# Optimization experiments

Hardware: AMD Instinct MI355X
Metric: run time of the kernel (lower is better)

Reference implementation:

```python
import jax, jax.numpy as jnp
import numpy as np

B, S, D = 64, 2048, 1024

def setup_inputs() -> dict:
    key = jax.random.key(0)
    k1, k2, k3 = jax.random.split(key, 3)
    enc_mask = jax.random.randint(k1, (B, S), 0, 2).astype(bool)  # True = masked (padding)
    enc_out = jax.random.normal(k2, (B, S, D), dtype=jnp.float32)
    dec_hid = jax.random.normal(k3, (B, D), dtype=jnp.float32)
    return {"enc_mask": enc_mask, "enc_out": enc_out, "dec_hid": dec_hid}

def reference(enc_mask, enc_out, dec_hid):
    # scores: [B, S] = dot(enc_out[b,s,:], dec_hid[b,:])
    sims = jnp.einsum('bsd,bd->bs', enc_out, dec_hid)
    sims = jnp.where(enc_mask, -jnp.inf, sims)
    attention = jax.nn.softmax(sims, axis=1)          # [B, S]
    context = jnp.einsum('bs,bsd->bd', attention, enc_out)  # [B, D]
    return context
```

## Files before the change

### kernel.cpp

```cpp
#include <hip/hip_runtime.h>
#include <math.h>


constexpr int Bc = 64;
constexpr int Sc = 2048;
constexpr int Dc = 1024;

__global__ __launch_bounds__(256, 4)
void attn_partial(const int* __restrict__ mask,
                  const float* __restrict__ enc,
                  const float* __restrict__ hid,
                  float* __restrict__ o_part,
                  float* __restrict__ ml_part,
                  float* __restrict__ out_final,
                  int SPLIT, int CHUNK)
{
    __shared__ float so[4][Dc];
    __shared__ float sm[4], sl[4];

    const int split = blockIdx.x;
    const int b     = blockIdx.y;
    const int tid   = threadIdx.x;
    const int wid   = tid >> 6;
    const int lane  = tid & 63;
    const int d0    = lane << 2;

    const float* hb = hid + (size_t)b * Dc;
    const float4 h0 = *(const float4*)(hb + d0);
    const float4 h1 = *(const float4*)(hb + d0 + 256);
    const float4 h2 = *(const float4*)(hb + d0 + 512);
    const float4 h3 = *(const float4*)(hb + d0 + 768);

    float4 o0 = make_float4(0.f,0.f,0.f,0.f);
    float4 o1 = o0, o2 = o0, o3 = o0;
    float m = -INFINITY, l = 0.f;

    const int rpw  = CHUNK >> 2;
    const int sbeg = split * CHUNK + wid * rpw;
    const int* mrow = mask + (size_t)b * Sc;
    const float* ebase = enc + ((size_t)b * Sc + (size_t)sbeg) * Dc;

    for (int i = 0; i < rpw; ++i) {
        if (mrow[sbeg + i]) continue;
        const float* row = ebase + (size_t)i * Dc;
        const float4 x0 = *(const float4*)(row + d0);
        const float4 x1 = *(const float4*)(row + d0 + 256);
        const float4 x2 = *(const float4*)(row + d0 + 512);
        const float4 x3 = *(const float4*)(row + d0 + 768);

        float p = x0.x*h0.x + x0.y*h0.y + x0.z*h0.z + x0.w*h0.w;
        p      += x1.x*h1.x + x1.y*h1.y + x1.z*h1.z + x1.w*h1.w;
        p      += x2.x*h2.x + x2.y*h2.y + x2.z*h2.z + x2.w*h2.w;
        p      += x3.x*h3.x + x3.y*h3.y + x3.z*h3.z + x3.w*h3.w;
        #pragma unroll
        for (int off = 32; off > 0; off >>= 1)
            p += __shfl_xor(p, off, 64);

        const float mn = fmaxf(m, p);
        const float a  = __expf(m - mn);
        const float w  = __expf(p - mn);
        l = l * a + w;
        m = mn;
        o0.x = o0.x*a + w*x0.x;  o0.y = o0.y*a + w*x0.y;
        o0.z = o0.z*a + w*x0.z;  o0.w = o0.w*a + w*x0.w;
        o1.x = o1.x*a + w*x1.x;  o1.y = o1.y*a + w*x1.y;
        o1.z = o1.z*a + w*x1.z;  o1.w = o1.w*a + w*x1.w;
        o2.x = o2.x*a + w*x2.x;  o2.y = o2.y*a + w*x2.y;
        o2.z = o2.z*a + w*x2.z;  o2.w = o2.w*a + w*x2.w;
        o3.x = o3.x*a + w*x3.x;  o3.y = o3.y*a + w*x3.y;
        o3.z = o3.z*a + w*x3.z;  o3.w = o3.w*a + w*x3.w;
    }

    if (lane == 0) { sm[wid] = m; sl[wid] = l; }
    *(float4*)&so[wid][d0      ] = o0;
    *(float4*)&so[wid][d0 + 256] = o1;
    *(float4*)&so[wid][d0 + 512] = o2;
    *(float4*)&so[wid][d0 + 768] = o3;
    __syncthreads();

    const float M  = fmaxf(fmaxf(sm[0], sm[1]), fmaxf(sm[2], sm[3]));
    const float e0 = __expf(sm[0] - M);
    const float e1 = __expf(sm[1] - M);
    const float e2 = __expf(sm[2] - M);
    const float e3 = __expf(sm[3] - M);
    const float L  = sl[0]*e0 + sl[1]*e1 + sl[2]*e2 + sl[3]*e3;

    const int dd = tid << 2;
    const float4 v0 = *(float4*)&so[0][dd];
    const float4 v1 = *(float4*)&so[1][dd];
    const float4 v2 = *(float4*)&so[2][dd];
    const float4 v3 = *(float4*)&so[3][dd];
    float4 acc;
    acc.x = v0.x*e0 + v1.x*e1 + v2.x*e2 + v3.x*e3;
    acc.y = v0.y*e0 + v1.y*e1 + v2.y*e2 + v3.y*e3;
    acc.z = v0.z*e0 + v1.z*e1 + v2.z*e2 + v3.z*e3;
    acc.w = v0.w*e0 + v1.w*e1 + v2.w*e2 + v3.w*e3;

    if (out_final) {
        const float inv = (L > 0.f) ? 1.f / L : 0.f;
        acc.x *= inv; acc.y *= inv; acc.z *= inv; acc.w *= inv;
        *(float4*)&out_final[(size_t)b * Dc + dd] = acc;
    } else {
        *(float4*)&o_part[((size_t)b * SPLIT + split) * Dc + dd] = acc;
        if (tid == 0) {
            ml_part[((size_t)b * SPLIT + split) * 2    ] = M;
            ml_part[((size_t)b * SPLIT + split) * 2 + 1] = L;
        }
    }
}

__global__ __launch_bounds__(256)
void attn_combine(const float* __restrict__ o_part,
                  const float* __restrict__ ml_part,
                  float* __restrict__ out, int SPLIT)
{
    __shared__ float sme[64], sle[64];
    const int b   = blockIdx.x;
    const int tid = threadIdx.x;
    if (tid < SPLIT) {
        sme[tid] = ml_part[((size_t)b * SPLIT + tid) * 2];
        sle[tid] = ml_part[((size_t)b * SPLIT + tid) * 2 + 1];
    }
    __syncthreads();

    float M = -INFINITY;
    for (int s = 0; s < SPLIT; ++s) M = fmaxf(M, sme[s]);
    float L = 0.f;
    for (int s = 0; s < SPLIT; ++s) L += sle[s] * __expf(sme[s] - M);

    const int dd = tid << 2;
    float4 acc = make_float4(0.f,0.f,0.f,0.f);
    for (int s = 0; s < SPLIT; ++s) {
        const float e = __expf(sme[s] - M);
        const float4 v = *(const float4*)&o_part[((size_t)b * SPLIT + s) * Dc + dd];
        acc.x += e * v.x; acc.y += e * v.y; acc.z += e * v.z; acc.w += e * v.w;
    }
    const float inv = (L > 0.f) ? 1.f / L : 0.f;
    acc.x *= inv; acc.y *= inv; acc.z *= inv; acc.w *= inv;
    *(float4*)&out[(size_t)b * Dc + dd] = acc;
}

extern "C" void kernel_launch(void* const* d_in, const int* in_sizes, int n_in,
                              void* d_out, int out_size, void* d_ws, size_t ws_size,
                              hipStream_t stream)
{
    const int*   mask = (const int*)d_in[0];
    const float* enc  = (const float*)d_in[1];
    const float* hid  = (const float*)d_in[2];
    float*       out  = (float*)d_out;

    int SPLIT = 32;
    while (SPLIT > 1 &&
           (size_t)Bc * SPLIT * (Dc + 2) * sizeof(float) > ws_size)
        SPLIT >>= 1;
    const bool direct =
        (SPLIT == 1) || ((size_t)Bc * (Dc + 2) * sizeof(float) > ws_size);
    if (direct) SPLIT = 1;

    float* o_part  = (float*)d_ws;
    float* ml_part = o_part + (size_t)Bc * SPLIT * Dc;

    attn_partial<<<dim3(SPLIT, Bc), 256, 0, stream>>>(
        mask, enc, hid,
        direct ? nullptr : o_part,
        direct ? nullptr : ml_part,
        direct ? out : nullptr,
        SPLIT, Sc / SPLIT);

    if (!direct)
        attn_combine<<<Bc, 256, 0, stream>>>(o_part, ml_part, out, SPLIT);
}
```

Baseline: 644.6 us.

## Batch four unmasked rows per iteration using ballot-compacted mask

After: 644.9 us. No clear change (+0.1%).

```diff
diff --git a/kernel.cpp b/kernel.cpp
--- a/kernel.cpp
+++ b/kernel.cpp
@@ -6,7 +6,19 @@
 constexpr int Sc = 2048;
 constexpr int Dc = 1024;
 
-__global__ __launch_bounds__(256, 4)
+__device__ __forceinline__ float dot16(const float4& a, const float4& b,
+                                       const float4& c, const float4& d,
+                                       const float4& h0, const float4& h1,
+                                       const float4& h2, const float4& h3)
+{
+    float p = a.x*h0.x + a.y*h0.y + a.z*h0.z + a.w*h0.w;
+    p      += b.x*h1.x + b.y*h1.y + b.z*h1.z + b.w*h1.w;
+    p      += c.x*h2.x + c.y*h2.y + c.z*h2.z + c.w*h2.w;
+    p      += d.x*h3.x + d.y*h3.y + d.z*h3.z + d.w*h3.w;
+    return p;
+}
+
+__global__ __launch_bounds__(256, 3)
 void attn_partial(const int* __restrict__ mask,
                   const float* __restrict__ enc,
                   const float* __restrict__ hid,
@@ -37,38 +49,80 @@
 
     const int rpw  = CHUNK >> 2;
     const int sbeg = split * CHUNK + wid * rpw;
-    const int* mrow = mask + (size_t)b * Sc;
+    const int* mrow = mask + (size_t)b * Sc + sbeg;
     const float* ebase = enc + ((size_t)b * Sc + (size_t)sbeg) * Dc;
 
-    for (int i = 0; i < rpw; ++i) {
-        if (mrow[sbeg + i]) continue;
-        const float* row = ebase + (size_t)i * Dc;
-        const float4 x0 = *(const float4*)(row + d0);
-        const float4 x1 = *(const float4*)(row + d0 + 256);
-        const float4 x2 = *(const float4*)(row + d0 + 512);
-        const float4 x3 = *(const float4*)(row + d0 + 768);
-
-        float p = x0.x*h0.x + x0.y*h0.y + x0.z*h0.z + x0.w*h0.w;
-        p      += x1.x*h1.x + x1.y*h1.y + x1.z*h1.z + x1.w*h1.w;
-        p      += x2.x*h2.x + x2.y*h2.y + x2.z*h2.z + x2.w*h2.w;
-        p      += x3.x*h3.x + x3.y*h3.y + x3.z*h3.z + x3.w*h3.w;
-        #pragma unroll
-        for (int off = 32; off > 0; off >>= 1)
-            p += __shfl_xor(p, off, 64);
-
-        const float mn = fmaxf(m, p);
-        const float a  = __expf(m - mn);
-        const float w  = __expf(p - mn);
-        l = l * a + w;
-        m = mn;
-        o0.x = o0.x*a + w*x0.x;  o0.y = o0.y*a + w*x0.y;
-        o0.z = o0.z*a + w*x0.z;  o0.w = o0.w*a + w*x0.w;
-        o1.x = o1.x*a + w*x1.x;  o1.y = o1.y*a + w*x1.y;
-        o1.z = o1.z*a + w*x1.z;  o1.w = o1.w*a + w*x1.w;
-        o2.x = o2.x*a + w*x2.x;  o2.y = o2.y*a + w*x2.y;
-        o2.z = o2.z*a + w*x2.z;  o2.w = o2.w*a + w*x2.w;
-        o3.x = o3.x*a + w*x3.x;  o3.y = o3.y*a + w*x3.y;
-        o3.z = o3.z*a + w*x3.z;  o3.w = o3.w*a + w*x3.w;
+    for (int w0 = 0; w0 < rpw; w0 += 64) {
+        const int nrem = rpw - w0;
+        const int nwin = nrem < 64 ? nrem : 64;
+        uint64_t bm = __ballot(lane < nwin && mrow[w0 + lane] == 0);
+
+        while (bm) {
+            const int r0 = __builtin_ctzll(bm); bm &= bm - 1;
+            int r1 = r0, r2 = r0, r3 = r0;
+            bool v1 = false, v2 = false, v3 = false;
+            if (bm) { v1 = true; r1 = __builtin_ctzll(bm); bm &= bm - 1; }
+            if (bm) { v2 = true; r2 = __builtin_ctzll(bm); bm &= bm - 1; }
+            if (bm) { v3 = true; r3 = __builtin_ctzll(bm); bm &= bm - 1; }
+
+            const float* R0 = ebase + (size_t)(w0 + r0) * Dc + d0;
+            const float* R1 = ebase + (size_t)(w0 + r1) * Dc + d0;
+            const float* R2 = ebase + (size_t)(w0 + r2) * Dc + d0;
+            const float* R3 = ebase + (size_t)(w0 + r3) * Dc + d0;
+
+            const float4 A0 = *(const float4*)(R0);       const float4 A1 = *(const float4*)(R0 + 256);
+            const float4 A2 = *(const float4*)(R0 + 512); const float4 A3 = *(const float4*)(R0 + 768);
+            const float4 B0 = *(const float4*)(R1);       const float4 B1 = *(const float4*)(R1 + 256);
+            const float4 B2 = *(const float4*)(R1 + 512); const float4 B3 = *(const float4*)(R1 + 768);
+            const float4 C0 = *(const float4*)(R2);       const float4 C1 = *(const float4*)(R2 + 256);
+            const float4 C2 = *(const float4*)(R2 + 512); const float4 C3 = *(const float4*)(R2 + 768);
+            const float4 D0 = *(const float4*)(R3);       const float4 D1 = *(const float4*)(R3 + 256);
+            const float4 D2 = *(const float4*)(R3 + 512); const float4 D3 = *(const float4*)(R3 + 768);
+
+            float p0 = dot16(A0,A1,A2,A3, h0,h1,h2,h3);
+            float p1 = dot16(B0,B1,B2,B3, h0,h1,h2,h3);
+            float p2 = dot16(C0,C1,C2,C3, h0,h1,h2,h3);
+            float p3 = dot16(D0,D1,D2,D3, h0,h1,h2,h3);
+
+            #pragma unroll
+            for (int off = 32; off > 0; off >>= 1) {
+                p0 += __shfl_xor(p0, off, 64);
+                p1 += __shfl_xor(p1, off, 64);
+                p2 += __shfl_xor(p2, off, 64);
+                p3 += __shfl_xor(p3, off, 64);
+            }
+
+            if (!v1) p1 = -INFINITY;
+            if (!v2) p2 = -INFINITY;
+            if (!v3) p3 = -INFINITY;
+
+            const float pm = fmaxf(fmaxf(p0, p1), fmaxf(p2, p3));
+            const float mn = fmaxf(m, pm);
+            const float al = __expf(m - mn);
+            const float e0 = __expf(p0 - mn);
+            const float e1 = __expf(p1 - mn);
+            const float e2 = __expf(p2 - mn);
+            const float e3 = __expf(p3 - mn);
+            m = mn;
+            l = l * al + (e0 + e1 + e2 + e3);
+
+            o0.x = o0.x*al + e0*A0.x + e1*B0.x + e2*C0.x + e3*D0.x;
+            o0.y = o0.y*al + e0*A0.y + e1*B0.y + e2*C0.y + e3*D0.y;
+            o0.z = o0.z*al + e0*A0.z + e1*B0.z + e2*C0.z + e3*D0.z;
+            o0.w = o0.w*al + e0*A0.w + e1*B0.w + e2*C0.w + e3*D0.w;
+            o1.x = o1.x*al + e0*A1.x + e1*B1.x + e2*C1.x + e3*D1.x;
+            o1.y = o1.y*al + e0*A1.y + e1*B1.y + e2*C1.y + e3*D1.y;
+            o1.z = o1.z*al + e0*A1.z + e1*B1.z + e2*C1.z + e3*D1.z;
+            o1.w = o1.w*al + e0*A1.w + e1*B1.w + e2*C1.w + e3*D1.w;
+            o2.x = o2.x*al + e0*A2.x + e1*B2.x + e2*C2.x + e3*D2.x;
+            o2.y = o2.y*al + e0*A2.y + e1*B2.y + e2*C2.y + e3*D2.y;
+            o2.z = o2.z*al + e0*A2.z + e1*B2.z + e2*C2.z + e3*D2.z;
+            o2.w = o2.w*al + e0*A2.w + e1*B2.w + e2*C2.w + e3*D2.w;
+            o3.x = o3.x*al + e0*A3.x + e1*B3.x + e2*C3.x + e3*D3.x;
+            o3.y = o3.y*al + e0*A3.y + e1*B3.y + e2*C3.y + e3*D3.y;
+            o3.z = o3.z*al + e0*A3.z + e1*B3.z + e2*C3.z + e3*D3.z;
+            o3.w = o3.w*al + e0*A3.w + e1*B3.w + e2*C3.w + e3*D3.w;
+        }
     }
 
     if (lane == 0) { sm[wid] = m; sl[wid] = l; }
@@ -79,10 +133,10 @@
     __syncthreads();
 
     const float M  = fmaxf(fmaxf(sm[0], sm[1]), fmaxf(sm[2], sm[3]));
-    const float e0 = __expf(sm[0] - M);
-    const float e1 = __expf(sm[1] - M);
-    const float e2 = __expf(sm[2] - M);
-    const float e3 = __expf(sm[3] - M);
+    const float e0 = (sm[0] == -INFINITY) ? 0.f : __expf(sm[0] - M);
+    const float e1 = (sm[1] == -INFINITY) ? 0.f : __expf(sm[1] - M);
+    const float e2 = (sm[2] == -INFINITY) ? 0.f : __expf(sm[2] - M);
+    const float e3 = (sm[3] == -INFINITY) ? 0.f : __expf(sm[3] - M);
     const float L  = sl[0]*e0 + sl[1]*e1 + sl[2]*e2 + sl[3]*e3;
 
     const int dd = tid << 2;
@@ -109,13 +163,14 @@
     }
 }
 
-__global__ __launch_bounds__(256)
+__global__ __launch_bounds__(64)
 void attn_combine(const float* __restrict__ o_part,
                   const float* __restrict__ ml_part,
                   float* __restrict__ out, int SPLIT)
 {
     __shared__ float sme[64], sle[64];
-    const int b   = blockIdx.x;
+    const int b   = blockIdx.y;
+    const int q   = blockIdx.x;
     const int tid = threadIdx.x;
     if (tid < SPLIT) {
         sme[tid] = ml_part[((size_t)b * SPLIT + tid) * 2];
@@ -126,12 +181,13 @@
     float M = -INFINITY;
     for (int s = 0; s < SPLIT; ++s) M = fmaxf(M, sme[s]);
     float L = 0.f;
-    for (int s = 0; s < SPLIT; ++s) L += sle[s] * __expf(sme[s] - M);
-
-    const int dd = tid << 2;
+    for (int s = 0; s < SPLIT; ++s)
+        L += (sme[s] == -INFINITY) ? 0.f : sle[s] * __expf(sme[s] - M);
+
+    const int dd = q * 256 + (tid << 2);
     float4 acc = make_float4(0.f,0.f,0.f,0.f);
     for (int s = 0; s < SPLIT; ++s) {
-        const float e = __expf(sme[s] - M);
+        const float e = (sme[s] == -INFINITY) ? 0.f : __expf(sme[s] - M);
         const float4 v = *(const float4*)&o_part[((size_t)b * SPLIT + s) * Dc + dd];
         acc.x += e * v.x; acc.y += e * v.y; acc.z += e * v.z; acc.w += e * v.w;
     }
@@ -168,5 +224,5 @@
         SPLIT, Sc / SPLIT);
 
     if (!direct)
-        attn_combine<<<Bc, 256, 0, stream>>>(o_part, ml_part, out, SPLIT);
-}
+        attn_combine<<<dim3(4, Bc), 64, 0, stream>>>(o_part, ml_part, out, SPLIT);
+}
```
